# Kernel optimization log

Measured on AMD Instinct MI355X. Metric: run time of the kernel, lower is better.

## Reference

```python
import jax, jax.numpy as jnp
import numpy as np

B, LATENT, P, NUM_ATOMS, H, L, E = 16, 128, 16, 64, 64, 4, 32768
N = P * NUM_ATOMS  # 1024

def _lin(k, i, o, s=0.05):
    kw, kb = jax.random.split(k)
    return jax.random.normal(kw, (i, o), jnp.float32) * s, jax.random.normal(kb, (o,), jnp.float32) * s

def setup_inputs() -> dict:
    key = jax.random.key(0)
    ks = jax.random.split(key, 32)
    z = jax.random.normal(ks[0], (B, LATENT), jnp.float32)
    edge_index = jax.random.randint(ks[1], (2, E), 0, N, jnp.int32)
    # build_node_features: (frame/P, atom/num_atoms, 1) per node
    fr = jnp.repeat(jnp.arange(P), NUM_ATOMS) / P
    at = jnp.tile(jnp.arange(NUM_ATOMS), P) / NUM_ATOMS
    node_features = jnp.stack([fr, at, jnp.ones(N)], -1).astype(jnp.float32)
    Wg, bg = _lin(ks[2], LATENT, H)
    Wn, bn = _lin(ks[3], 3, H)
    def stack(fn, base):
        outs = [fn(jax.random.fold_in(key, base + l)) for l in range(L)]
        return tuple(jnp.stack(t) for t in zip(*outs))
    eW1, eb1 = stack(lambda k: _lin(k, 2 * H + 1, H), 100)
    eW2, eb2 = stack(lambda k: _lin(k, H, H), 200)
    cW1, cb1 = stack(lambda k: _lin(k, H, H), 300)
    cW2 = jnp.stack([jax.random.normal(jax.random.fold_in(key, 400 + l), (H, 1), jnp.float32) * 0.05 for l in range(L)])
    nW1, nb1 = stack(lambda k: _lin(k, 2 * H, H), 500)
    nW2, nb2 = stack(lambda k: _lin(k, H, H), 600)
    lng = jnp.ones((L, H), jnp.float32)
    lnb = jnp.zeros((L, H), jnp.float32)
    oW1, ob1 = _lin(ks[4], H, H)
    oW2, ob2 = _lin(ks[5], H, 3)
    return dict(z=z, edge_index=edge_index, node_features=node_features, Wg=Wg, bg=bg, Wn=Wn, bn=bn,
                eW1=eW1, eb1=eb1, eW2=eW2, eb2=eb2, cW1=cW1, cb1=cb1, cW2=cW2,
                nW1=nW1, nb1=nb1, nW2=nW2, nb2=nb2, lng=lng, lnb=lnb,
                oW1=oW1, ob1=ob1, oW2=oW2, ob2=ob2)

def _forward(z, edge_index, node_features, Wg, bg, Wn, bn, eW1, eb1, eW2, eb2,
             cW1, cb1, cW2, nW1, nb1, nW2, nb2, lng, lnb, oW1, ob1, oW2, ob2):
    b = z.shape[0]
    n = node_features.shape[0]
    row, col = edge_index[0], edge_index[1]  # aggregate messages to row
    counts = jnp.clip(jnp.zeros((n,), jnp.float32).at[row].add(1.0), 1.0, None)
    g = z @ Wg + bg                              # [B,H]
    h = (node_features @ Wn + bn)[None] + g[:, None]  # [B,N,H]
    pos = jnp.zeros((b, n, 3), h.dtype)
    for l in range(L):
        hi, hj = h[:, row], h[:, col]            # [B,E,H] gathers
        diff = pos[:, row] - pos[:, col]         # [B,E,3]
        d2 = jnp.sum(diff * diff, -1, keepdims=True)
        m = jax.nn.silu(jnp.concatenate([hi, hj, d2], -1) @ eW1[l] + eb1[l])
        m = jax.nn.silu(m @ eW2[l] + eb2[l])     # [B,E,H]
        w = jax.nn.silu(m @ cW1[l] + cb1[l]) @ cW2[l]  # [B,E,1]
        trans = diff * w
        pos = pos + jnp.zeros_like(pos).at[:, row].add(trans) / counts[None, :, None]
        agg = jnp.zeros_like(h).at[:, row].add(m)      # scatter-sum to nodes
        u = jax.nn.silu(jnp.concatenate([h, agg], -1) @ nW1[l] + nb1[l]) @ nW2[l] + nb2[l]
        h = h + u                                 # node residual
        mu = jnp.mean(h, -1, keepdims=True)
        var = jnp.mean((h - mu) ** 2, -1, keepdims=True)
        h = (h - mu) * jax.lax.rsqrt(var + 1e-5) * lng[l] + lnb[l]
    out = jax.nn.relu(h @ oW1 + ob1) @ oW2 + ob2   # [B,N,3]
    return out.reshape(b, -1)

def reference(z, edge_index, node_features, Wg, bg, Wn, bn, eW1, eb1, eW2, eb2,
              cW1, cb1, cW2, nW1, nb1, nW2, nb2, lng, lnb, oW1, ob1, oW2, ob2):
    return _forward(z, edge_index, node_features, Wg, bg, Wn, bn, eW1, eb1, eW2, eb2,
                    cW1, cb1, cW2, nW1, nb1, nW2, nb2, lng, lnb, oW1, ob1, oW2, ob2)
```

## Files before the change

kernel.cpp:

```cpp
#include <hip/hip_runtime.h>
#include <hip/hip_bf16.h>


namespace {

constexpr int kE = 32768, kLat = 128;

typedef __attribute__((ext_vector_type(8))) short short8;
typedef __attribute__((ext_vector_type(4))) float floatx4;

__device__ __forceinline__ unsigned short f2bf(float f){
  union { float f; unsigned int u; } v; v.f = f;
  unsigned int r = v.u + 0x7fffu + ((v.u >> 16) & 1u);
  return (unsigned short)(r >> 16);
}
__device__ __forceinline__ unsigned int packbf(float a, float b){
  return ((unsigned int)f2bf(b) << 16) | (unsigned int)f2bf(a);
}
__device__ __forceinline__ unsigned int pack2f(float a, float b){
  unsigned int ua = __float_as_uint(a) + 0x8000u;
  unsigned int ub = __float_as_uint(b) + 0x8000u;
  return __builtin_amdgcn_perm(ub, ua, 0x07060302);
}
__device__ __forceinline__ float bflo(unsigned int u){
  union { unsigned int u; float f; } v; v.u = u << 16; return v.f;
}
__device__ __forceinline__ float bfhi(unsigned int u){
  union { unsigned int u; float f; } v; v.u = u & 0xffff0000u; return v.f;
}
__device__ __forceinline__ float silu2(float x){
  float u = __builtin_amdgcn_exp2f(-1.44269504f * x);
  return x * __builtin_amdgcn_rcpf(1.0f + u);
}

__device__ __forceinline__ void stageU(float* Wl, const float* src, int u){
  const float4* p = (const float4*)src;
  float4* d = (float4*)Wl;
  #pragma unroll
  for (int q = 0; q < 8; q++) d[u + q*128] = p[u + q*128];
}
__device__ __forceinline__ void gemm32(const float* Wl, const float* Xl,
                                       int j0, int r0, float acc[4][4]){
  #pragma unroll 4
  for (int k = 0; k < 64; k++){
    float4 w = *(const float4*)(Wl + k*64 + j0);
    float4 x = *(const float4*)(Xl + k*36 + r0);
    float xv[4] = { x.x, x.y, x.z, x.w };
    float wv[4] = { w.x, w.y, w.z, w.w };
    #pragma unroll
    for (int i = 0; i < 4; i++)
      #pragma unroll
      for (int j = 0; j < 4; j++)
        acc[i][j] += xv[i]*wv[j];
  }
}

__global__ void k_scancnt(const int* ei, int* off, int* fill,
                          const float* z, const float* Wg, const float* bg,
                          float* g){
  __shared__ int s0[1024];
  __shared__ int s1[1024];
  int t = threadIdx.x;
  s0[t] = 0; fill[t] = 0;
  __syncthreads();
  #pragma unroll
  for (int i = 0; i < 32; i++) atomicAdd(&s0[ei[i*1024 + t]], 1);
  __syncthreads();
  int c = s0[t];
  int* src = s0; int* dst = s1;
  for (int o = 1; o < 1024; o <<= 1){
    int v = src[t] + ((t >= o) ? src[t-o] : 0);
    dst[t] = v; __syncthreads();
    int* tmp = src; src = dst; dst = tmp;
  }
  int inc = src[t];
  off[t] = inc - c;
  if (t == 1023) off[1024] = inc;
  int b = t >> 6, j = t & 63;
  float acc = bg[j];
  for (int k = 0; k < kLat; k++) acc += z[b*kLat + k] * Wg[k*64 + j];
  g[b*64 + j] = acc;
}

__global__ void k_bucket(const int* ei, const int* off, int* fill, int* ecol,
                         const float* eW2, unsigned short* wfragE,
                         const float* nf, const float* Wn, const float* bn,
                         const float* eW1, const float* eb1, const float* g,
                         float* An1, float* An2, float* Ag1, float* Ag2){
  __shared__ __align__(16) float W0[4096];
  __shared__ __align__(16) float W1[4096];
  __shared__ __align__(16) float HR[16*68];
  int tid = threadIdx.x, bid = blockIdx.x;
  int e = bid*256 + tid;
  int r = ei[e];
  int s = atomicAdd(&fill[r], 1);
  ecol[off[r] + s] = ei[kE + e];
  if (bid < 4){
    int l = bid;
    for (int i = tid; i < 4096; i += 256){
      int f = i >> 9, lane = (i >> 3) & 63, j8 = i & 7;
      int jt = f >> 1, ks = f & 1;
      int k = ks*32 + (lane >> 4)*8 + j8;
      int j = jt*16 + (lane & 15);
      wfragE[l*4096 + i] = f2bf(eW2[l*4096 + k*64 + j]);
    }
  } else if (bid < 68){
    const float4* e1a = (const float4*)(eW1);
    const float4* e1b = (const float4*)(eW1 + 4096);
    for (int i = tid; i < 1024; i += 256){
      ((float4*)W0)[i] = e1a[i]; ((float4*)W1)[i] = e1b[i];
    }
    int rl = tid >> 4, c = tid & 15, j0 = c*4;
    int n = (bid - 4)*16 + rl;
    float f0 = nf[n*3], f1 = nf[n*3+1], f2 = nf[n*3+2];
    float4 hv;
    hv.x = f0*Wn[j0+0] + f1*Wn[64+j0+0] + f2*Wn[128+j0+0] + bn[j0+0];
    hv.y = f0*Wn[j0+1] + f1*Wn[64+j0+1] + f2*Wn[128+j0+1] + bn[j0+1];
    hv.z = f0*Wn[j0+2] + f1*Wn[64+j0+2] + f2*Wn[128+j0+2] + bn[j0+2];
    hv.w = f0*Wn[j0+3] + f1*Wn[64+j0+3] + f2*Wn[128+j0+3] + bn[j0+3];
    *(float4*)(HR + rl*68 + j0) = hv;
    __syncthreads();
    float4 b1 = *(const float4*)(eb1 + j0);
    float a1[4] = { b1.x, b1.y, b1.z, b1.w };
    float a2[4] = { 0.f, 0.f, 0.f, 0.f };
    #pragma unroll 8
    for (int k = 0; k < 64; k++){
      float hk = HR[rl*68 + k];
      float4 w1 = *(const float4*)(W0 + k*64 + j0);
      float4 w2 = *(const float4*)(W1 + k*64 + j0);
      a1[0] += hk*w1.x; a1[1] += hk*w1.y; a1[2] += hk*w1.z; a1[3] += hk*w1.w;
      a2[0] += hk*w2.x; a2[1] += hk*w2.y; a2[2] += hk*w2.z; a2[3] += hk*w2.w;
    }
    float4 o1 = { a1[0], a1[1], a1[2], a1[3] };
    float4 o2 = { a2[0], a2[1], a2[2], a2[3] };
    *(float4*)(An1 + n*64 + j0) = o1;
    *(float4*)(An2 + n*64 + j0) = o2;
  } else if (bid == 68){
    int bb = tid >> 4, j0 = (tid & 15)*4;
    float a1[4] = {0.f,0.f,0.f,0.f}, a2[4] = {0.f,0.f,0.f,0.f};
    for (int k = 0; k < 64; k++){
      float gk = g[bb*64 + k];
      float4 w1 = *(const float4*)(eW1 + k*64 + j0);
      float4 w2 = *(const float4*)(eW1 + 4096 + k*64 + j0);
      a1[0] += gk*w1.x; a1[1] += gk*w1.y; a1[2] += gk*w1.z; a1[3] += gk*w1.w;
      a2[0] += gk*w2.x; a2[1] += gk*w2.y; a2[2] += gk*w2.z; a2[3] += gk*w2.w;
    }
    float4 o1 = { a1[0], a1[1], a1[2], a1[3] };
    float4 o2 = { a2[0], a2[1], a2[2], a2[3] };
    *(float4*)(Ag1 + bb*64 + j0) = o1;
    *(float4*)(Ag2 + bb*64 + j0) = o2;
  }
}

__global__ __launch_bounds__(256, 1) void k_pre1(const float* nf, const float* Wn,
      const float* bn, const float* g, const float* An1, const float* An2,
      const float* Ag1, const float* Ag2, float* h, float* A1,
      unsigned short* A2){
  int idx = blockIdx.x*256 + threadIdx.x;
  int row = idx >> 4;
  int j0  = (idx & 15) * 4;
  int n = row >> 4, bb = row & 15;
  float4 a1 = *(const float4*)(An1 + n*64 + j0);
  float4 g1 = *(const float4*)(Ag1 + bb*64 + j0);
  a1.x += g1.x; a1.y += g1.y; a1.z += g1.z; a1.w += g1.w;
  *(float4*)(A1 + row*64 + j0) = a1;
  float4 a2 = *(const float4*)(An2 + n*64 + j0);
  float4 g2 = *(const float4*)(Ag2 + bb*64 + j0);
  a2.x += g2.x; a2.y += g2.y; a2.z += g2.z; a2.w += g2.w;
  uint2 pk; pk.x = packbf(a2.x, a2.y); pk.y = packbf(a2.z, a2.w);
  *(uint2*)(A2 + row*64 + j0) = pk;
  float f0 = nf[n*3], f1 = nf[n*3+1], f2 = nf[n*3+2];
  float4 w0 = *(const float4*)(Wn + j0);
  float4 w1 = *(const float4*)(Wn + 64 + j0);
  float4 w2 = *(const float4*)(Wn + 128 + j0);
  float4 bv = *(const float4*)(bn + j0);
  float4 gv = *(const float4*)(g + bb*64 + j0);
  float4 hv;
  hv.x = f0*w0.x + f1*w1.x + f2*w2.x + bv.x + gv.x;
  hv.y = f0*w0.y + f1*w1.y + f2*w2.y + bv.y + gv.y;
  hv.z = f0*w0.z + f1*w1.z + f2*w2.z + bv.z + gv.z;
  hv.w = f0*w0.w + f1*w1.w + f2*w2.w + bv.w + gv.w;
  *(float4*)(h + (bb*1024 + n)*64 + j0) = hv;
}

template <bool LAST>
__global__ __launch_bounds__(256) void k_layer(int l,
      const float* A1r, const unsigned short* A2r,
      float* A1w, unsigned short* A2w,
      float* h, const unsigned short* wfragE, const float* eb2,
      const int* off, const int* ecol,
      const float* nW1, const float* nb1_, const float* nW2, const float* nb2_,
      const float* lng_, const float* lnb_, const float* eW1, const float* eb1_,
      const float* oW1, const float* ob1_, const float* oW2, const float* ob2_,
      float* out){
  __shared__ __align__(16) float Wa[4096];
  __shared__ __align__(16) float Wb[4096];
  __shared__ __align__(16) float XT[64*36];
  __shared__ __align__(16) float AGL[64*36];
  __shared__ float W2o[192];
  __shared__ float ob2s[4];
  int tid = threadIdx.x, bid = blockIdx.x;
  int n0 = bid * 2;
  int lane = tid & 63, wv = tid >> 6, m = lane & 15, quad = lane >> 4;

  for (int i = tid; i < 64*36; i += 256) AGL[i] = 0.f;
  __syncthreads();

  {
    int nd = n0 + (wv >> 1);
    short8 wf[8];
    #pragma unroll
    for (int f = 0; f < 8; f++)
      wf[f] = *(const short8*)(wfragE + l*4096 + f*512 + lane*8);
    floatx4 dini[4], agg[4];
    #pragma unroll
    for (int jt = 0; jt < 4; jt++){
      dini[jt] = *(const floatx4*)(eb2 + l*64 + jt*16 + quad*4);
      agg[jt] = (floatx4){0.f,0.f,0.f,0.f};
    }
    int e0 = off[nd] + (wv & 1), e1 = off[nd+1];
    if (e0 < e1){
      float4 a1[4];
      #pragma unroll
      for (int ks = 0; ks < 2; ks++){
        a1[ks*2+0] = *(const float4*)(A1r + (nd<<10) + (m<<6) + ks*32 + quad*8);
        a1[ks*2+1] = *(const float4*)(A1r + (nd<<10) + (m<<6) + ks*32 + quad*8 + 4);
      }
      int c0 = ecol[e0];
      uint4 p0 = *(const uint4*)(A2r + ((c0<<4)+m)*64 + quad*8);
      uint4 p1 = *(const uint4*)(A2r + ((c0<<4)+m)*64 + 32 + quad*8);
      for (int e = e0; e < e1; e += 2){
        uint4 c_0 = p0, c_1 = p1;
        if (e + 2 < e1){
          int cn = ecol[e+2];
          p0 = *(const uint4*)(A2r + ((cn<<4)+m)*64 + quad*8);
          p1 = *(const uint4*)(A2r + ((cn<<4)+m)*64 + 32 + quad*8);
        }
        short8 bfr[2];
        #pragma unroll
        for (int ks = 0; ks < 2; ks++){
          uint4 a2r = (ks == 0) ? c_0 : c_1;
          float4 x0 = a1[ks*2+0];
          float4 x1 = a1[ks*2+1];
          float v0 = silu2(x0.x + bflo(a2r.x));
          float v1 = silu2(x0.y + bfhi(a2r.x));
          float v2 = silu2(x0.z + bflo(a2r.y));
          float v3 = silu2(x0.w + bfhi(a2r.y));
          float v4 = silu2(x1.x + bflo(a2r.z));
          float v5 = silu2(x1.y + bfhi(a2r.z));
          float v6 = silu2(x1.z + bflo(a2r.w));
          float v7 = silu2(x1.w + bfhi(a2r.w));
          union { uint4 u; short8 s; } bu;
          bu.u.x = pack2f(v0, v1); bu.u.y = pack2f(v2, v3);
          bu.u.z = pack2f(v4, v5); bu.u.w = pack2f(v6, v7);
          bfr[ks] = bu.s;
        }
        #pragma unroll
        for (int jt = 0; jt < 4; jt++){
          floatx4 d = dini[jt];
          d = __builtin_amdgcn_mfma_f32_16x16x32_bf16(wf[jt*2+0], bfr[0], d, 0, 0, 0);
          d = __builtin_amdgcn_mfma_f32_16x16x32_bf16(wf[jt*2+1], bfr[1], d, 0, 0, 0);
          floatx4 a = agg[jt];
          a.x += silu2(d.x); a.y += silu2(d.y);
          a.z += silu2(d.z); a.w += silu2(d.w);
          agg[jt] = a;
        }
      }
    }
    int rloc = (wv >> 1)*16 + m;
    #pragma unroll
    for (int jt = 0; jt < 4; jt++)
      #pragma unroll
      for (int i = 0; i < 4; i++)
        atomicAdd(&AGL[(jt*16 + quad*4 + i)*36 + rloc], agg[jt][i]);
  }

  bool lo = (tid < 128);
  int up = tid - 128;
  int c = tid & 15, gq = tid >> 4;
  int j0 = c*4, r0 = gq*4;

  float hold[4][4];
  float acc[4][4];
  if (lo){
    #pragma unroll
    for (int i = 0; i < 4; i++){
      int rr = r0 + i;
      int nd2 = n0 + (rr >> 4), bb = rr & 15;
      float4 v = *(const float4*)(h + (bb*1024 + nd2)*64 + j0);
      hold[i][0]=v.x; hold[i][1]=v.y; hold[i][2]=v.z; hold[i][3]=v.w;
    }
    #pragma unroll
    for (int j = 0; j < 4; j++){
      float4 t = { hold[0][j], hold[1][j], hold[2][j], hold[3][j] };
      *(float4*)(XT + (j0 + j)*36 + r0) = t;
    }
    float4 b1 = *(const float4*)(nb1_ + l*64 + j0);
    float bv[4] = { b1.x, b1.y, b1.z, b1.w };
    #pragma unroll
    for (int i = 0; i < 4; i++)
      #pragma unroll
      for (int j = 0; j < 4; j++) acc[i][j] = bv[j];
  } else {
    stageU(Wa, nW1 + l*8192, up);
  }
  __syncthreads();
  if (lo) gemm32(Wa, XT, j0, r0, acc);
  else    stageU(Wb, nW1 + l*8192 + 4096, up);
  __syncthreads();
  if (lo){
    gemm32(Wb, AGL, j0, r0, acc);
    #pragma unroll
    for (int i = 0; i < 4; i++)
      #pragma unroll
      for (int j = 0; j < 4; j++) acc[i][j] = silu2(acc[i][j]);
    #pragma unroll
    for (int j = 0; j < 4; j++){
      float4 t = { acc[0][j], acc[1][j], acc[2][j], acc[3][j] };
      *(float4*)(XT + (j0 + j)*36 + r0) = t;
    }
  } else {
    stageU(Wa, nW2 + l*4096, up);
  }
  __syncthreads();
  float hn[4][4];
  if (lo){
    float u4[4][4];
    float4 b2 = *(const float4*)(nb2_ + l*64 + j0);
    float bv[4] = { b2.x, b2.y, b2.z, b2.w };
    #pragma unroll
    for (int i = 0; i < 4; i++)
      #pragma unroll
      for (int j = 0; j < 4; j++) u4[i][j] = bv[j];
    gemm32(Wa, XT, j0, r0, u4);
    float4 lgv = *(const float4*)(lng_ + l*64 + j0);
    float4 lbv = *(const float4*)(lnb_ + l*64 + j0);
    #pragma unroll
    for (int i = 0; i < 4; i++){
      float hv[4];
      #pragma unroll
      for (int j = 0; j < 4; j++) hv[j] = hold[i][j] + u4[i][j];
      float s1 = hv[0]+hv[1]+hv[2]+hv[3];
      float s2 = hv[0]*hv[0]+hv[1]*hv[1]+hv[2]*hv[2]+hv[3]*hv[3];
      s1 += __shfl_xor(s1, 1, 64); s1 += __shfl_xor(s1, 2, 64);
      s1 += __shfl_xor(s1, 4, 64); s1 += __shfl_xor(s1, 8, 64);
      s2 += __shfl_xor(s2, 1, 64); s2 += __shfl_xor(s2, 2, 64);
      s2 += __shfl_xor(s2, 4, 64); s2 += __shfl_xor(s2, 8, 64);
      float mu  = s1 * (1.0f/64.0f);
      float var = s2 * (1.0f/64.0f) - mu*mu;
      float rs  = rsqrtf(var + 1e-5f);
      hn[i][0] = (hv[0]-mu)*rs*lgv.x + lbv.x;
      hn[i][1] = (hv[1]-mu)*rs*lgv.y + lbv.y;
      hn[i][2] = (hv[2]-mu)*rs*lgv.z + lbv.z;
      hn[i][3] = (hv[3]-mu)*rs*lgv.w + lbv.w;
    }
    if (!LAST){
      #pragma unroll
      for (int i = 0; i < 4; i++){
        int rr = r0 + i;
        int nd2 = n0 + (rr >> 4), bb = rr & 15;
        float4 v = { hn[i][0], hn[i][1], hn[i][2], hn[i][3] };
        *(float4*)(h + (bb*1024 + nd2)*64 + j0) = v;
      }
    }
    #pragma unroll
    for (int j = 0; j < 4; j++){
      float4 t = { hn[0][j], hn[1][j], hn[2][j], hn[3][j] };
      *(float4*)(AGL + (j0 + j)*36 + r0) = t;
    }
  } else {
    if (!LAST){
      stageU(Wb, eW1 + (l+1)*8256, up);
    } else {
      stageU(Wb, oW1, up);
      W2o[up] = oW2[up];
      if (up < 64) W2o[128 + up] = oW2[128 + up];
      if (up < 3)  ob2s[up] = ob2_[up];
    }
  }
  __syncthreads();
  if (!LAST){
    float a1r[4][4];
    if (lo){
      float4 b1 = *(const float4*)(eb1_ + (l+1)*64 + j0);
      float bv[4] = { b1.x, b1.y, b1.z, b1.w };
      #pragma unroll
      for (int i = 0; i < 4; i++)
        #pragma unroll
        for (int j = 0; j < 4; j++) a1r[i][j] = bv[j];
      gemm32(Wb, AGL, j0, r0, a1r);
    } else {
      stageU(Wa, eW1 + (l+1)*8256 + 4096, up);
    }
    __syncthreads();
    if (lo){
      float a2r[4][4];
      #pragma unroll
      for (int i = 0; i < 4; i++)
        #pragma unroll
        for (int j = 0; j < 4; j++) a2r[i][j] = 0.f;
      gemm32(Wa, AGL, j0, r0, a2r);
      #pragma unroll
      for (int i = 0; i < 4; i++){
        int rr = r0 + i;
        int nd2 = n0 + (rr >> 4), bb = rr & 15;
        int tb = (nd2*16 + bb)*64 + j0;
        float4 o1 = { a1r[i][0], a1r[i][1], a1r[i][2], a1r[i][3] };
        *(float4*)(A1w + tb) = o1;
        uint2 pk; pk.x = packbf(a2r[i][0], a2r[i][1]);
        pk.y = packbf(a2r[i][2], a2r[i][3]);
        *(uint2*)(A2w + tb) = pk;
      }
    }
  } else {
    if (lo){
      float tr[4][4];
      float4 b1 = *(const float4*)(ob1_ + j0);
      float bv[4] = { b1.x, b1.y, b1.z, b1.w };
      #pragma unroll
      for (int i = 0; i < 4; i++)
        #pragma unroll
        for (int j = 0; j < 4; j++) tr[i][j] = bv[j];
      gemm32(Wb, AGL, j0, r0, tr);
      #pragma unroll
      for (int i = 0; i < 4; i++)
        #pragma unroll
        for (int j = 0; j < 4; j++) tr[i][j] = fmaxf(tr[i][j], 0.f);
      float po[4][3];
      #pragma unroll
      for (int i = 0; i < 4; i++){ po[i][0]=0.f; po[i][1]=0.f; po[i][2]=0.f; }
      #pragma unroll
      for (int j = 0; j < 4; j++){
        float w0 = W2o[(j0+j)*3 + 0];
        float w1 = W2o[(j0+j)*3 + 1];
        float w2 = W2o[(j0+j)*3 + 2];
        #pragma unroll
        for (int i = 0; i < 4; i++){
          po[i][0] += tr[i][j]*w0;
          po[i][1] += tr[i][j]*w1;
          po[i][2] += tr[i][j]*w2;
        }
      }
      #pragma unroll
      for (int i = 0; i < 4; i++)
        #pragma unroll
        for (int uu = 0; uu < 3; uu++){
          float v = po[i][uu];
          v += __shfl_xor(v, 1, 64); v += __shfl_xor(v, 2, 64);
          v += __shfl_xor(v, 4, 64); v += __shfl_xor(v, 8, 64);
          po[i][uu] = v;
        }
      if (c == 0){
        #pragma unroll
        for (int i = 0; i < 4; i++){
          int rr = r0 + i;
          int nd2 = n0 + (rr >> 4), bb = rr & 15;
          out[bb*3072 + nd2*3 + 0] = po[i][0] + ob2s[0];
          out[bb*3072 + nd2*3 + 1] = po[i][1] + ob2s[1];
          out[bb*3072 + nd2*3 + 2] = po[i][2] + ob2s[2];
        }
      }
    }
  }
}

}

extern "C" void kernel_launch(void* const* d_in, const int* in_sizes, int n_in,
                              void* d_out, int out_size, void* d_ws, size_t ws_size,
                              hipStream_t stream){
  const float* z   = (const float*)d_in[0];
  const int*   ei  = (const int*)d_in[1];
  const float* nf  = (const float*)d_in[2];
  const float* Wg  = (const float*)d_in[3];  const float* bg  = (const float*)d_in[4];
  const float* Wn  = (const float*)d_in[5];  const float* bn  = (const float*)d_in[6];
  const float* eW1 = (const float*)d_in[7];  const float* eb1 = (const float*)d_in[8];
  const float* eW2 = (const float*)d_in[9];  const float* eb2 = (const float*)d_in[10];
  const float* nW1 = (const float*)d_in[14]; const float* nb1 = (const float*)d_in[15];
  const float* nW2 = (const float*)d_in[16]; const float* nb2 = (const float*)d_in[17];
  const float* lng = (const float*)d_in[18]; const float* lnb = (const float*)d_in[19];
  const float* oW1 = (const float*)d_in[20]; const float* ob1 = (const float*)d_in[21];
  const float* oW2 = (const float*)d_in[22]; const float* ob2 = (const float*)d_in[23];

  float* W      = (float*)d_ws;
  float* h      = W;
  float* A1a    = W + 1048576;
  float* A1b    = W + 2097152;
  unsigned short* A2a    = (unsigned short*)(W + 3145728);
  unsigned short* A2b    = (unsigned short*)(W + 3670016);
  unsigned short* wfragE = (unsigned short*)(W + 4194304);
  float* g      = W + 4202496;
  float* An1    = W + 4203520;
  float* An2    = W + 4269056;
  float* Ag1    = W + 4334592;
  float* Ag2    = W + 4335616;
  int*   off    = (int*)(W + 4336640);
  int*   fill   = off + 1025;
  int*   ecol   = fill + 1024;

  k_scancnt<<<1, 1024, 0, stream>>>(ei, off, fill, z, Wg, bg, g);
  k_bucket <<<128, 256, 0, stream>>>(ei, off, fill, ecol, eW2, wfragE,
                                     nf, Wn, bn, eW1, eb1, g, An1, An2, Ag1, Ag2);
  k_pre1   <<<1024,256, 0, stream>>>(nf, Wn, bn, g, An1, An2, Ag1, Ag2, h, A1a, A2a);

  for (int l = 0; l < 4; l++){
    const float* A1r = (l & 1) ? A1b : A1a;
    const unsigned short* A2r = (l & 1) ? A2b : A2a;
    float* A1w = (l & 1) ? A1a : A1b;
    unsigned short* A2w = (l & 1) ? A2a : A2b;
    if (l < 3)
      k_layer<false><<<512, 256, 0, stream>>>(l, A1r, A2r, A1w, A2w, h, wfragE,
            eb2, off, ecol, nW1, nb1, nW2, nb2, lng, lnb, eW1, eb1,
            oW1, ob1, oW2, ob2, (float*)d_out);
    else
      k_layer<true> <<<512, 256, 0, stream>>>(l, A1r, A2r, A1w, A2w, h, wfragE,
            eb2, off, ecol, nW1, nb1, nW2, nb2, lng, lnb, eW1, eb1,
            oW1, ob1, oW2, ob2, (float*)d_out);
  }
}
```

Baseline: 335.1 us.

## Assign one node per block with four waves splitting its edges

The layer kernel now runs one destination node per block instead of two, with 1024 blocks, and all four waves stride over that node's edges in steps of four. The node-update GEMMs shrink to 16 rows handled by a single wave while the other three waves stage weights, and the transposed shared buffers shrink to match. The goal is more parallelism and better balance of the edge-aggregation phase across the GPU. In exchange, weight staging into shared memory is repeated twice as often across the grid, and only one wave does the dense node math.

```diff
diff --git a/kernel.cpp b/kernel.cpp
--- a/kernel.cpp
+++ b/kernel.cpp
@@ -33,18 +33,17 @@
   return x * __builtin_amdgcn_rcpf(1.0f + u);
 }
 
-__device__ __forceinline__ void stageU(float* Wl, const float* src, int u){
+__device__ __forceinline__ void stage192(float* Wl, const float* src, int u){
   const float4* p = (const float4*)src;
   float4* d = (float4*)Wl;
-  #pragma unroll
-  for (int q = 0; q < 8; q++) d[u + q*128] = p[u + q*128];
-}
-__device__ __forceinline__ void gemm32(const float* Wl, const float* Xl,
+  for (int i = u; i < 1024; i += 192) d[i] = p[i];
+}
+__device__ __forceinline__ void gemm16(const float* Wl, const float* Xl,
                                        int j0, int r0, float acc[4][4]){
   #pragma unroll 4
   for (int k = 0; k < 64; k++){
     float4 w = *(const float4*)(Wl + k*64 + j0);
-    float4 x = *(const float4*)(Xl + k*36 + r0);
+    float4 x = *(const float4*)(Xl + k*20 + r0);
     float xv[4] = { x.x, x.y, x.z, x.w };
     float wv[4] = { w.x, w.y, w.z, w.w };
     #pragma unroll
@@ -195,19 +194,17 @@
       float* out){
   __shared__ __align__(16) float Wa[4096];
   __shared__ __align__(16) float Wb[4096];
-  __shared__ __align__(16) float XT[64*36];
-  __shared__ __align__(16) float AGL[64*36];
+  __shared__ __align__(16) float XT[64*20];
+  __shared__ __align__(16) float AGL[64*20];
   __shared__ float W2o[192];
   __shared__ float ob2s[4];
-  int tid = threadIdx.x, bid = blockIdx.x;
-  int n0 = bid * 2;
+  int tid = threadIdx.x, nd = blockIdx.x;
   int lane = tid & 63, wv = tid >> 6, m = lane & 15, quad = lane >> 4;
 
-  for (int i = tid; i < 64*36; i += 256) AGL[i] = 0.f;
+  for (int i = tid; i < 64*20; i += 256) AGL[i] = 0.f;
   __syncthreads();
 
   {
-    int nd = n0 + (wv >> 1);
     short8 wf[8];
     #pragma unroll
     for (int f = 0; f < 8; f++)
@@ -218,7 +215,7 @@
       dini[jt] = *(const floatx4*)(eb2 + l*64 + jt*16 + quad*4);
       agg[jt] = (floatx4){0.f,0.f,0.f,0.f};
     }
-    int e0 = off[nd] + (wv & 1), e1 = off[nd+1];
+    int e0 = off[nd] + wv, e1 = off[nd+1];
     if (e0 < e1){
       float4 a1[4];
       #pragma unroll
@@ -229,10 +226,10 @@
       int c0 = ecol[e0];
       uint4 p0 = *(const uint4*)(A2r + ((c0<<4)+m)*64 + quad*8);
       uint4 p1 = *(const uint4*)(A2r + ((c0<<4)+m)*64 + 32 + quad*8);
-      for (int e = e0; e < e1; e += 2){
+      for (int e = e0; e < e1; e += 4){
         uint4 c_0 = p0, c_1 = p1;
-        if (e + 2 < e1){
-          int cn = ecol[e+2];
+        if (e + 4 < e1){
+          int cn = ecol[e+4];
           p0 = *(const uint4*)(A2r + ((cn<<4)+m)*64 + quad*8);
           p1 = *(const uint4*)(A2r + ((cn<<4)+m)*64 + 32 + quad*8);
         }
@@ -267,17 +264,16 @@
         }
       }
     }
-    int rloc = (wv >> 1)*16 + m;
     #pragma unroll
     for (int jt = 0; jt < 4; jt++)
       #pragma unroll
       for (int i = 0; i < 4; i++)
-        atomicAdd(&AGL[(jt*16 + quad*4 + i)*36 + rloc], agg[jt][i]);
-  }
-
-  bool lo = (tid < 128);
-  int up = tid - 128;
-  int c = tid & 15, gq = tid >> 4;
+        atomicAdd(&AGL[(jt*16 + quad*4 + i)*20 + m], agg[jt][i]);
+  }
+
+  bool lo = (wv == 0);
+  int up = tid - 64;
+  int c = tid & 15, gq = (tid >> 4) & 3;
   int j0 = c*4, r0 = gq*4;
 
   float hold[4][4];
@@ -285,15 +281,14 @@
   if (lo){
     #pragma unroll
     for (int i = 0; i < 4; i++){
-      int rr = r0 + i;
-      int nd2 = n0 + (rr >> 4), bb = rr & 15;
-      float4 v = *(const float4*)(h + (bb*1024 + nd2)*64 + j0);
+      int bb = r0 + i;
+      float4 v = *(const float4*)(h + (bb*1024 + nd)*64 + j0);
       hold[i][0]=v.x; hold[i][1]=v.y; hold[i][2]=v.z; hold[i][3]=v.w;
     }
     #pragma unroll
     for (int j = 0; j < 4; j++){
       float4 t = { hold[0][j], hold[1][j], hold[2][j], hold[3][j] };
-      *(float4*)(XT + (j0 + j)*36 + r0) = t;
+      *(float4*)(XT + (j0 + j)*20 + r0) = t;
     }
     float4 b1 = *(const float4*)(nb1_ + l*64 + j0);
     float bv[4] = { b1.x, b1.y, b1.z, b1.w };
@@ -302,14 +297,14 @@
       #pragma unroll
       for (int j = 0; j < 4; j++) acc[i][j] = bv[j];
   } else {
-    stageU(Wa, nW1 + l*8192, up);
-  }
-  __syncthreads();
-  if (lo) gemm32(Wa, XT, j0, r0, acc);
-  else    stageU(Wb, nW1 + l*8192 + 4096, up);
+    stage192(Wa, nW1 + l*8192, up);
+  }
+  __syncthreads();
+  if (lo) gemm16(Wa, XT, j0, r0, acc);
+  else    stage192(Wb, nW1 + l*8192 + 4096, up);
   __syncthreads();
   if (lo){
-    gemm32(Wb, AGL, j0, r0, acc);
+    gemm16(Wb, AGL, j0, r0, acc);
     #pragma unroll
     for (int i = 0; i < 4; i++)
       #pragma unroll
@@ -317,10 +312,10 @@
     #pragma unroll
     for (int j = 0; j < 4; j++){
       float4 t = { acc[0][j], acc[1][j], acc[2][j], acc[3][j] };
-      *(float4*)(XT + (j0 + j)*36 + r0) = t;
+      *(float4*)(XT + (j0 + j)*20 + r0) = t;
     }
   } else {
-    stageU(Wa, nW2 + l*4096, up);
+    stage192(Wa, nW2 + l*4096, up);
   }
   __syncthreads();
   float hn[4][4];
@@ -332,7 +327,7 @@
     for (int i = 0; i < 4; i++)
       #pragma unroll
       for (int j = 0; j < 4; j++) u4[i][j] = bv[j];
-    gemm32(Wa, XT, j0, r0, u4);
+    gemm16(Wa, XT, j0, r0, u4);
     float4 lgv = *(const float4*)(lng_ + l*64 + j0);
     float4 lbv = *(const float4*)(lnb_ + l*64 + j0);
     #pragma unroll
@@ -357,25 +352,23 @@
     if (!LAST){
       #pragma unroll
       for (int i = 0; i < 4; i++){
-        int rr = r0 + i;
-        int nd2 = n0 + (rr >> 4), bb = rr & 15;
+        int bb = r0 + i;
         float4 v = { hn[i][0], hn[i][1], hn[i][2], hn[i][3] };
-        *(float4*)(h + (bb*1024 + nd2)*64 + j0) = v;
+        *(float4*)(h + (bb*1024 + nd)*64 + j0) = v;
       }
     }
     #pragma unroll
     for (int j = 0; j < 4; j++){
       float4 t = { hn[0][j], hn[1][j], hn[2][j], hn[3][j] };
-      *(float4*)(AGL + (j0 + j)*36 + r0) = t;
+      *(float4*)(XT + (j0 + j)*20 + r0) = t;
     }
   } else {
     if (!LAST){
-      stageU(Wb, eW1 + (l+1)*8256, up);
+      stage192(Wb, eW1 + (l+1)*8256, up);
     } else {
-      stageU(Wb, oW1, up);
-      W2o[up] = oW2[up];
-      if (up < 64) W2o[128 + up] = oW2[128 + up];
-      if (up < 3)  ob2s[up] = ob2_[up];
+      stage192(Wb, oW1, up);
+      if (up < 192) W2o[up] = oW2[up];
+      if (up < 3)   ob2s[up] = ob2_[up];
     }
   }
   __syncthreads();
@@ -388,9 +381,9 @@
       for (int i = 0; i < 4; i++)
         #pragma unroll
         for (int j = 0; j < 4; j++) a1r[i][j] = bv[j];
-      gemm32(Wb, AGL, j0, r0, a1r);
+      gemm16(Wb, XT, j0, r0, a1r);
     } else {
-      stageU(Wa, eW1 + (l+1)*8256 + 4096, up);
+      stage192(Wa, eW1 + (l+1)*8256 + 4096, up);
     }
     __syncthreads();
     if (lo){
@@ -399,12 +392,11 @@
       for (int i = 0; i < 4; i++)
         #pragma unroll
         for (int j = 0; j < 4; j++) a2r[i][j] = 0.f;
-      gemm32(Wa, AGL, j0, r0, a2r);
+      gemm16(Wa, XT, j0, r0, a2r);
       #pragma unroll
       for (int i = 0; i < 4; i++){
-        int rr = r0 + i;
-        int nd2 = n0 + (rr >> 4), bb = rr & 15;
-        int tb = (nd2*16 + bb)*64 + j0;
+        int bb = r0 + i;
+        int tb = (nd*16 + bb)*64 + j0;
         float4 o1 = { a1r[i][0], a1r[i][1], a1r[i][2], a1r[i][3] };
         *(float4*)(A1w + tb) = o1;
         uint2 pk; pk.x = packbf(a2r[i][0], a2r[i][1]);
@@ -421,7 +413,7 @@
       for (int i = 0; i < 4; i++)
         #pragma unroll
         for (int j = 0; j < 4; j++) tr[i][j] = bv[j];
-      gemm32(Wb, AGL, j0, r0, tr);
+      gemm16(Wb, XT, j0, r0, tr);
       #pragma unroll
       for (int i = 0; i < 4; i++)
         #pragma unroll
@@ -453,11 +445,10 @@
       if (c == 0){
         #pragma unroll
         for (int i = 0; i < 4; i++){
-          int rr = r0 + i;
-          int nd2 = n0 + (rr >> 4), bb = rr & 15;
-          out[bb*3072 + nd2*3 + 0] = po[i][0] + ob2s[0];
-          out[bb*3072 + nd2*3 + 1] = po[i][1] + ob2s[1];
-          out[bb*3072 + nd2*3 + 2] = po[i][2] + ob2s[2];
+          int bb = r0 + i;
+          out[bb*3072 + nd*3 + 0] = po[i][0] + ob2s[0];
+          out[bb*3072 + nd*3 + 1] = po[i][1] + ob2s[1];
+          out[bb*3072 + nd*3 + 2] = po[i][2] + ob2s[2];
         }
       }
     }
@@ -509,11 +500,11 @@
     float* A1w = (l & 1) ? A1a : A1b;
     unsigned short* A2w = (l & 1) ? A2a : A2b;
     if (l < 3)
-      k_layer<false><<<512, 256, 0, stream>>>(l, A1r, A2r, A1w, A2w, h, wfragE,
+      k_layer<false><<<1024, 256, 0, stream>>>(l, A1r, A2r, A1w, A2w, h, wfragE,
             eb2, off, ecol, nW1, nb1, nW2, nb2, lng, lnb, eW1, eb1,
             oW1, ob1, oW2, ob2, (float*)d_out);
     else
-      k_layer<true> <<<512, 256, 0, stream>>>(l, A1r, A2r, A1w, A2w, h, wfragE,
+      k_layer<true> <<<1024, 256, 0, stream>>>(l, A1r, A2r, A1w, A2w, h, wfragE,
             eb2, off, ecol, nW1, nb1, nW2, nb2, lng, lnb, eW1, eb1,
             oW1, ob1, oW2, ob2, (float*)d_out);
   }
```

After: 428.2 us. +27.8%, slower.
